# Performance work log

Measured on AMD Instinct MI355X. Metric: run time of the kernel, lower is better.

## Reference

```python
import jax, jax.numpy as jnp
import numpy as np

BERT_DIM = 768
N_ROWS = 5
N_COLS = 12
LN_EPS = 1e-5


def setup_inputs() -> dict:
    key = jax.random.key(0)
    ks = jax.random.split(key, 12)
    B, S = 256, 512
    token_hidden = jax.random.normal(ks[0], (B, S, BERT_DIM), dtype=jnp.float32)
    attention_mask = jax.random.randint(ks[1], (B, S), 0, 2, dtype=jnp.int32)
    s = lambda fan_in: 1.0 / np.sqrt(fan_in)
    return {
        "token_hidden": token_hidden,
        "attention_mask": attention_mask,
        # token_attention: Linear(768,128) -> Tanh -> Linear(128,1)
        "att_w1": jax.random.normal(ks[2], (128, BERT_DIM), dtype=jnp.float32) * s(BERT_DIM),
        "att_b1": jnp.zeros((128,), dtype=jnp.float32),
        "att_w2": jax.random.normal(ks[3], (1, 128), dtype=jnp.float32) * s(128),
        "att_b2": jnp.zeros((1,), dtype=jnp.float32),
        # feature_projector: Linear(768,256) -> GELU -> Dropout(eval) -> Linear(256,5)
        "proj_w1": jax.random.normal(ks[4], (256, BERT_DIM), dtype=jnp.float32) * s(BERT_DIM),
        "proj_b1": jnp.zeros((256,), dtype=jnp.float32),
        "proj_w2": jax.random.normal(ks[5], (N_ROWS, 256), dtype=jnp.float32) * s(256),
        "proj_b2": jnp.zeros((N_ROWS,), dtype=jnp.float32),
        # LayerNorm([5, 12])
        "ln_gamma": jnp.ones((N_ROWS, N_COLS), dtype=jnp.float32),
        "ln_beta": jnp.zeros((N_ROWS, N_COLS), dtype=jnp.float32),
    }


def reference(token_hidden, attention_mask, att_w1, att_b1, att_w2, att_b2,
              proj_w1, proj_b1, proj_w2, proj_b2, ln_gamma, ln_beta):
    # token attention scores: [B, S]
    h = jnp.tanh(jnp.einsum("bsd,hd->bsh", token_hidden, att_w1) + att_b1)
    scores = (jnp.einsum("bsh,oh->bso", h, att_w2) + att_b2)[..., 0]
    scores = jnp.where(attention_mask == 0, jnp.finfo(scores.dtype).min, scores)
    weights = jax.nn.softmax(scores, axis=-1)
    # top-k token selection (indices sorted ascending to preserve order)
    k = min(N_COLS, token_hidden.shape[1])
    _, top_idx = jax.lax.top_k(weights, k)  # [B, k]
    top_idx = jnp.sort(top_idx, axis=-1)
    selected = jnp.take_along_axis(token_hidden, top_idx[:, :, None], axis=1)  # [B, k, D]
    # feature projector (dropout is eval no-op)
    f = jax.nn.gelu(jnp.einsum("bkd,hd->bkh", selected, proj_w1) + proj_b1, approximate=False)
    f = jnp.einsum("bkh,rh->bkr", f, proj_w2) + proj_b2  # [B, k, n_rows]
    features = jnp.transpose(f, (0, 2, 1))  # [B, n_rows, k]
    if features.shape[-1] < N_COLS:
        features = jnp.pad(features, ((0, 0), (0, 0), (0, N_COLS - features.shape[-1])))
    # LayerNorm over trailing [n_rows, n_cols]
    mean = jnp.mean(features, axis=(-2, -1), keepdims=True)
    var = jnp.var(features, axis=(-2, -1), keepdims=True)
    return ln_gamma * (features - mean) * jax.lax.rsqrt(var + LN_EPS) + ln_beta
```

## Files before the change

### kernel.cpp

```cpp
#include <hip/hip_runtime.h>
#include <math.h>

#define B_BATCH 256
#define S_LEN   512
#define D_DIM   768
#define H_ATT   128
#define TOPK    12
#define NCAND   16
#define H_PROJ  256
#define N_ROWS  5
#define N_COLS  12

typedef __bf16 bf16x8 __attribute__((ext_vector_type(8)));
typedef float  f32x4  __attribute__((ext_vector_type(4)));

#define WS_SCORES 0
#define WS_WHI    524288
#define WS_WLO    720896
#define WS_W1Q    917504
#define WS_W1P    1310720

__global__ __launch_bounds__(256) void prep_kernel(
    const float* __restrict__ w1,
    const float* __restrict__ pw1,
    __bf16* __restrict__ whi, __bf16* __restrict__ wlo,
    float* __restrict__ w1q, float* __restrict__ w1p)
{
    int id = blockIdx.x * 256 + threadIdx.x;
    if (id < 98304) {
        int j    = id & 7;
        int lane = (id >> 3) & 63;
        int rest = id >> 9;
        int kt   = rest % 24;
        int nt   = rest / 24;
        int n = nt * 16 + (lane & 15);
        int k = kt * 32 + (lane >> 4) * 8 + j;
        float f = w1[n * D_DIM + k];
        __bf16 h = (__bf16)f;
        whi[id] = h;
        wlo[id] = (__bf16)(f - (float)h);
    } else if (id < 196608) {
        int e2 = id - 98304;
        int i  = e2 & 3;
        int n  = (e2 >> 2) & 127;
        int k4 = e2 >> 9;
        w1q[e2] = w1[n * D_DIM + k4 * 4 + i];
    } else {
        int e  = id - 196608;
        int i  = e & 3;
        int j  = (e >> 2) & 255;
        int k4 = e >> 10;
        w1p[e] = pw1[j * D_DIM + k4 * 4 + i];
    }
}

__device__ inline void split8(float4 a, float4 b, bf16x8& hi, bf16x8& lo) {
    float v[8] = {a.x, a.y, a.z, a.w, b.x, b.y, b.z, b.w};
#pragma unroll
    for (int i = 0; i < 8; ++i) {
        __bf16 h = (__bf16)v[i];
        hi[i] = h;
        lo[i] = (__bf16)(v[i] - (float)h);
    }
}

__global__ __launch_bounds__(256) void score_mfma(
    const float*  __restrict__ th,
    const __bf16* __restrict__ whi,
    const __bf16* __restrict__ wlo,
    const float*  __restrict__ b1,
    const float*  __restrict__ w2,
    float* __restrict__ scores)
{
    const int ln = threadIdx.x & 63;
    const int gw = (blockIdx.x * 256 + threadIdx.x) >> 6;

    const size_t row0 = (size_t)gw * 32 + (ln & 15);
    const float* pa0 = th + row0 * D_DIM + (ln >> 4) * 8;
    const float* pa1 = pa0 + 16 * D_DIM;

    f32x4 acc[2][8];
    const f32x4 z = {0.f, 0.f, 0.f, 0.f};
#pragma unroll
    for (int i = 0; i < 2; ++i)
#pragma unroll
        for (int j = 0; j < 8; ++j) acc[i][j] = z;

    float4 c00 = *(const float4*)(pa0);
    float4 c01 = *(const float4*)(pa0 + 4);
    float4 c10 = *(const float4*)(pa1);
    float4 c11 = *(const float4*)(pa1 + 4);

    for (int kt = 0; kt < 24; ++kt) {
        const int ktn = (kt < 23) ? kt + 1 : 23;
        float4 n00 = *(const float4*)(pa0 + ktn * 32);
        float4 n01 = *(const float4*)(pa0 + ktn * 32 + 4);
        float4 n10 = *(const float4*)(pa1 + ktn * 32);
        float4 n11 = *(const float4*)(pa1 + ktn * 32 + 4);

        bf16x8 ah0, al0, ah1, al1;
        split8(c00, c01, ah0, al0);
        split8(c10, c11, ah1, al1);

        const __bf16* bhp = whi + ((size_t)kt * 64 + ln) * 8;
        const __bf16* blp = wlo + ((size_t)kt * 64 + ln) * 8;
#pragma unroll
        for (int nt = 0; nt < 8; ++nt) {
            bf16x8 bh = *(const bf16x8*)(bhp + (size_t)nt * 24 * 512);
            bf16x8 bl = *(const bf16x8*)(blp + (size_t)nt * 24 * 512);
            acc[0][nt] = __builtin_amdgcn_mfma_f32_16x16x32_bf16(ah0, bh, acc[0][nt], 0, 0, 0);
            acc[0][nt] = __builtin_amdgcn_mfma_f32_16x16x32_bf16(al0, bh, acc[0][nt], 0, 0, 0);
            acc[0][nt] = __builtin_amdgcn_mfma_f32_16x16x32_bf16(ah0, bl, acc[0][nt], 0, 0, 0);
            acc[1][nt] = __builtin_amdgcn_mfma_f32_16x16x32_bf16(ah1, bh, acc[1][nt], 0, 0, 0);
            acc[1][nt] = __builtin_amdgcn_mfma_f32_16x16x32_bf16(al1, bh, acc[1][nt], 0, 0, 0);
            acc[1][nt] = __builtin_amdgcn_mfma_f32_16x16x32_bf16(ah1, bl, acc[1][nt], 0, 0, 0);
        }
        c00 = n00; c01 = n01; c10 = n10; c11 = n11;
    }

    const int col = ln & 15;
    float b1v[8], w2v[8];
#pragma unroll
    for (int nt = 0; nt < 8; ++nt) {
        b1v[nt] = b1[nt * 16 + col];
        w2v[nt] = w2[nt * 16 + col];
    }
#pragma unroll
    for (int mf = 0; mf < 2; ++mf)
#pragma unroll
        for (int r = 0; r < 4; ++r) {
            float s = 0.f;
#pragma unroll
            for (int nt = 0; nt < 8; ++nt)
                s += tanhf(acc[mf][nt][r] + b1v[nt]) * w2v[nt];
            s += __shfl_xor(s, 1, 64);
            s += __shfl_xor(s, 2, 64);
            s += __shfl_xor(s, 4, 64);
            s += __shfl_xor(s, 8, 64);
            if (col == 0)
                scores[(size_t)gw * 32 + mf * 16 + (ln >> 4) * 4 + r] = s;
        }
}

__global__ __launch_bounds__(256) void select_kernel(
    const float* __restrict__ th,
    const int*   __restrict__ mask,
    const float* __restrict__ ascores,
    const float* __restrict__ w1q,
    const float* __restrict__ ab1,
    const float* __restrict__ aw2,
    const float* __restrict__ w1p,
    const float* __restrict__ pb1,
    const float* __restrict__ pw2,
    const float* __restrict__ pb2,
    const float* __restrict__ gamma,
    const float* __restrict__ beta,
    float* __restrict__ out)
{
    const int b   = blockIdx.x;
    const int tid = threadIdx.x;
    const int wv  = tid >> 6;
    const int ln  = tid & 63;

    __shared__ float4 xc[NCAND][192];
    __shared__ unsigned long long wtop[64];
    __shared__ int   cand[NCAND];
    __shared__ float redW[4][8];
    __shared__ float exact_sc[NCAND];
    __shared__ int   sel_slot[TOPK];
    __shared__ float gbuf[TOPK][H_PROJ + 1];
    __shared__ float feat[N_ROWS * N_COLS];
    __shared__ float stats[2];

    const float NEG_MIN = -3.402823466e38f;

    {
        int i0 = wv * 128 + ln, i1 = i0 + 64;
        float v0 = ascores[(size_t)b * S_LEN + i0];
        if (mask[(size_t)b * S_LEN + i0] == 0) v0 = NEG_MIN;
        float v1 = ascores[(size_t)b * S_LEN + i1];
        if (mask[(size_t)b * S_LEN + i1] == 0) v1 = NEG_MIN;
        unsigned k0 = __float_as_uint(v0);
        k0 = ((int)k0 >= 0) ? (k0 | 0x80000000u) : ~k0;
        unsigned k1 = __float_as_uint(v1);
        k1 = ((int)k1 >= 0) ? (k1 | 0x80000000u) : ~k1;
        unsigned long long p0 = ((unsigned long long)k0 << 32) | (0xFFFFFFFFu - (unsigned)i0);
        unsigned long long p1 = ((unsigned long long)k1 << 32) | (0xFFFFFFFFu - (unsigned)i1);
        for (int it = 0; it < NCAND; ++it) {
            unsigned long long m = p0 > p1 ? p0 : p1;
#pragma unroll
            for (int s = 1; s <= 32; s <<= 1) {
                unsigned long long o = __shfl_xor(m, s, 64);
                if (o > m) m = o;
            }
            if (ln == 0) wtop[wv * 16 + it] = m;
            if (p0 == m) p0 = 0ull;
            else if (p1 == m) p1 = 0ull;
        }
    }
    __syncthreads();
    if (wv == 0) {
        unsigned long long q = wtop[ln];
        for (int it = 0; it < NCAND; ++it) {
            unsigned long long m = q;
#pragma unroll
            for (int s = 1; s <= 32; s <<= 1) {
                unsigned long long o = __shfl_xor(m, s, 64);
                if (o > m) m = o;
            }
            if (ln == 0) cand[it] = (int)(0xFFFFFFFFu - (unsigned)(m & 0xFFFFFFFFu));
            if (q == m) q = 0ull;
        }
    }
    __syncthreads();

#pragma unroll
    for (int i = 0; i < 12; ++i) {
        int f = tid + 256 * i;
        int c = f / 192, k4 = f % 192;
        xc[c][k4] = *(const float4*)(th + ((size_t)b * S_LEN + cand[c]) * D_DIM + k4 * 4);
    }
    __syncthreads();

    {
        const int n = tid & 127;
        const int h = tid >> 7;
        float accs[8];
#pragma unroll
        for (int ci = 0; ci < 8; ++ci) accs[ci] = 0.f;
        for (int k4 = 0; k4 < 192; ++k4) {
            float4 w = *(const float4*)(w1q + (size_t)(k4 * 128 + n) * 4);
#pragma unroll
            for (int ci = 0; ci < 8; ++ci) {
                float4 x = xc[2 * ci + h][k4];
                accs[ci] += w.x * x.x + w.y * x.y + w.z * x.z + w.w * x.w;
            }
        }
        float b1n = ab1[n], w2n = aw2[n];
#pragma unroll
        for (int ci = 0; ci < 8; ++ci) {
            float val = tanhf(accs[ci] + b1n) * w2n;
            val += __shfl_xor(val, 1, 64);
            val += __shfl_xor(val, 2, 64);
            val += __shfl_xor(val, 4, 64);
            val += __shfl_xor(val, 8, 64);
            val += __shfl_xor(val, 16, 64);
            val += __shfl_xor(val, 32, 64);
            if (ln == 0) redW[wv][ci] = val;
        }
    }
    __syncthreads();
    if (tid < NCAND) {
        int c = tid;
        float ex = (c & 1) ? (redW[2][c >> 1] + redW[3][c >> 1])
                           : (redW[0][c >> 1] + redW[1][c >> 1]);
        if (mask[(size_t)b * S_LEN + cand[c]] == 0) ex = -INFINITY;
        exact_sc[c] = ex;
    }
    __syncthreads();

    if (tid == 0) {
        unsigned picked = 0;
        int slots[TOPK];
        for (int it = 0; it < TOPK; ++it) {
            float best = -INFINITY; int bslot = -1; int bidx = 1 << 30;
            for (int c = 0; c < NCAND; ++c) {
                if (picked & (1u << c)) continue;
                float e = exact_sc[c]; int idx = cand[c];
                if (e > best || (e == best && idx < bidx)) { best = e; bslot = c; bidx = idx; }
            }
            picked |= 1u << bslot;
            slots[it] = bslot;
        }
        for (int i = 1; i < TOPK; ++i) {
            int s = slots[i], key = cand[s], j = i - 1;
            while (j >= 0 && cand[slots[j]] > key) { slots[j + 1] = slots[j]; --j; }
            slots[j + 1] = s;
        }
        for (int t = 0; t < TOPK; ++t) sel_slot[t] = slots[t];
    }
    __syncthreads();

    {
        const int c0 = wv * 3;
        int s0 = sel_slot[c0], s1 = sel_slot[c0 + 1], s2 = sel_slot[c0 + 2];
        float accp[4][3];
#pragma unroll
        for (int cc = 0; cc < 4; ++cc) {
            float bj = pb1[cc * 64 + ln];
            accp[cc][0] = bj; accp[cc][1] = bj; accp[cc][2] = bj;
        }
        for (int k4 = 0; k4 < 192; ++k4) {
            float4 x0 = xc[s0][k4];
            float4 x1 = xc[s1][k4];
            float4 x2 = xc[s2][k4];
#pragma unroll
            for (int cc = 0; cc < 4; ++cc) {
                float4 w = *(const float4*)(w1p + (size_t)(k4 * 256 + cc * 64 + ln) * 4);
                accp[cc][0] += w.x * x0.x + w.y * x0.y + w.z * x0.z + w.w * x0.w;
                accp[cc][1] += w.x * x1.x + w.y * x1.y + w.z * x1.z + w.w * x1.w;
                accp[cc][2] += w.x * x2.x + w.y * x2.y + w.z * x2.z + w.w * x2.w;
            }
        }
#pragma unroll
        for (int cc = 0; cc < 4; ++cc)
#pragma unroll
            for (int c = 0; c < 3; ++c) {
                float hh = accp[cc][c];
                gbuf[c0 + c][cc * 64 + ln] =
                    0.5f * hh * (1.0f + erff(hh * 0.70710678118654752f));
            }
    }
    __syncthreads();

    if (tid < TOPK * N_ROWS) {
        int t = tid / N_ROWS, r = tid % N_ROWS;
        float s = pb2[r];
        for (int j = 0; j < H_PROJ; ++j) s += gbuf[t][j] * pw2[r * H_PROJ + j];
        feat[r * N_COLS + t] = s;
    }
    __syncthreads();

    if (tid == 0) {
        float sum = 0.f;
        for (int i = 0; i < N_ROWS * N_COLS; ++i) sum += feat[i];
        float mean = sum / 60.f;
        float sq = 0.f;
        for (int i = 0; i < N_ROWS * N_COLS; ++i) { float d = feat[i] - mean; sq += d * d; }
        stats[0] = mean;
        stats[1] = sq / 60.f;
    }
    __syncthreads();
    if (tid < N_ROWS * N_COLS) {
        float x = feat[tid];
        out[(size_t)b * 60 + tid] =
            gamma[tid] * (x - stats[0]) * rsqrtf(stats[1] + 1e-5f) + beta[tid];
    }
}

extern "C" void kernel_launch(void* const* d_in, const int* in_sizes, int n_in,
                              void* d_out, int out_size, void* d_ws, size_t ws_size,
                              hipStream_t stream) {
    const float* th   = (const float*)d_in[0];
    const int*   mask = (const int*)  d_in[1];
    const float* aw1  = (const float*)d_in[2];
    const float* ab1  = (const float*)d_in[3];
    const float* aw2  = (const float*)d_in[4];
    const float* pw1  = (const float*)d_in[6];
    const float* pb1  = (const float*)d_in[7];
    const float* pw2  = (const float*)d_in[8];
    const float* pb2  = (const float*)d_in[9];
    const float* gam  = (const float*)d_in[10];
    const float* bet  = (const float*)d_in[11];
    float* out = (float*)d_out;

    char* ws = (char*)d_ws;
    float*  scores = (float*)(ws + WS_SCORES);
    __bf16* whi    = (__bf16*)(ws + WS_WHI);
    __bf16* wlo    = (__bf16*)(ws + WS_WLO);
    float*  w1q    = (float*)(ws + WS_W1Q);
    float*  w1p    = (float*)(ws + WS_W1P);

    hipLaunchKernelGGL(prep_kernel, dim3(1536), dim3(256), 0, stream,
                       aw1, pw1, whi, wlo, w1q, w1p);
    hipLaunchKernelGGL(score_mfma, dim3(1024), dim3(256), 0, stream,
                       th, whi, wlo, ab1, aw2, scores);
    hipLaunchKernelGGL(select_kernel, dim3(B_BATCH), dim3(256), 0, stream,
                       th, mask, scores, w1q, ab1, aw2,
                       w1p, pb1, pw2, pb2, gam, bet, out);
}
```

Measured before the change: 792.5 us.

## Stage score-GEMM weights in LDS via async loads; retile projector loop

The score kernel now makes each 4-wave block cooperatively stage the bf16 hi/lo weight tiles into double-buffered LDS using global_load_lds. This replaces the per-wave global weight reads, so the four waves share one copy and global traffic for B drops. A block barrier is added every k-step, and launch bounds now request 4 blocks per CU. In the select kernel, each thread now owns one hidden unit across all 12 selected tokens, so every w1p weight is loaded once instead of once per wave. The second projection layer is vectorised with float4 reads, for which the gbuf padding is changed to keep rows 16-byte aligned.

```diff
diff --git a/kernel.cpp b/kernel.cpp
--- a/kernel.cpp
+++ b/kernel.cpp
@@ -13,6 +13,9 @@
 
 typedef __bf16 bf16x8 __attribute__((ext_vector_type(8)));
 typedef float  f32x4  __attribute__((ext_vector_type(4)));
+
+#define GLOBAL_AS __attribute__((address_space(1)))
+#define LDS_AS    __attribute__((address_space(3)))
 
 #define WS_SCORES 0
 #define WS_WHI    524288
@@ -64,7 +67,7 @@
     }
 }
 
-__global__ __launch_bounds__(256) void score_mfma(
+__global__ __launch_bounds__(256, 4) void score_mfma(
     const float*  __restrict__ th,
     const __bf16* __restrict__ whi,
     const __bf16* __restrict__ wlo,
@@ -72,12 +75,29 @@
     const float*  __restrict__ w2,
     float* __restrict__ scores)
 {
-    const int ln = threadIdx.x & 63;
-    const int gw = (blockIdx.x * 256 + threadIdx.x) >> 6;
-
-    const size_t row0 = (size_t)gw * 32 + (ln & 15);
+    __shared__ __bf16 Bs[2][2][8 * 512];
+
+    const int tid = threadIdx.x;
+    const int wv  = tid >> 6;
+    const int ln  = tid & 63;
+
+    const size_t row0 = (size_t)blockIdx.x * 128 + wv * 32 + (ln & 15);
     const float* pa0 = th + row0 * D_DIM + (ln >> 4) * 8;
     const float* pa1 = pa0 + 16 * D_DIM;
+
+    auto stage = [&](int kt, int buf) {
+#pragma unroll
+        for (int q = 0; q < 4; ++q) {
+            int s  = wv + q * 4;
+            int hl = s >> 3;
+            int nt = s & 7;
+            const __bf16* src = (hl ? wlo : whi) +
+                                (((size_t)nt * 24 + kt) * 64 + ln) * 8;
+            __bf16* dst = &Bs[buf][hl][nt * 512];
+            __builtin_amdgcn_global_load_lds(
+                (GLOBAL_AS const void*)src, (LDS_AS void*)dst, 16, 0, 0);
+        }
+    };
 
     f32x4 acc[2][8];
     const f32x4 z = {0.f, 0.f, 0.f, 0.f};
@@ -90,24 +110,28 @@
     float4 c01 = *(const float4*)(pa0 + 4);
     float4 c10 = *(const float4*)(pa1);
     float4 c11 = *(const float4*)(pa1 + 4);
+    stage(0, 0);
+    __syncthreads();
 
     for (int kt = 0; kt < 24; ++kt) {
-        const int ktn = (kt < 23) ? kt + 1 : 23;
-        float4 n00 = *(const float4*)(pa0 + ktn * 32);
-        float4 n01 = *(const float4*)(pa0 + ktn * 32 + 4);
-        float4 n10 = *(const float4*)(pa1 + ktn * 32);
-        float4 n11 = *(const float4*)(pa1 + ktn * 32 + 4);
+        const int buf = kt & 1;
+        float4 n00, n01, n10, n11;
+        if (kt < 23) {
+            n00 = *(const float4*)(pa0 + (kt + 1) * 32);
+            n01 = *(const float4*)(pa0 + (kt + 1) * 32 + 4);
+            n10 = *(const float4*)(pa1 + (kt + 1) * 32);
+            n11 = *(const float4*)(pa1 + (kt + 1) * 32 + 4);
+            stage(kt + 1, buf ^ 1);
+        }
 
         bf16x8 ah0, al0, ah1, al1;
         split8(c00, c01, ah0, al0);
         split8(c10, c11, ah1, al1);
 
-        const __bf16* bhp = whi + ((size_t)kt * 64 + ln) * 8;
-        const __bf16* blp = wlo + ((size_t)kt * 64 + ln) * 8;
 #pragma unroll
         for (int nt = 0; nt < 8; ++nt) {
-            bf16x8 bh = *(const bf16x8*)(bhp + (size_t)nt * 24 * 512);
-            bf16x8 bl = *(const bf16x8*)(blp + (size_t)nt * 24 * 512);
+            bf16x8 bh = *(bf16x8*)(&Bs[buf][0][nt * 512 + ln * 8]);
+            bf16x8 bl = *(bf16x8*)(&Bs[buf][1][nt * 512 + ln * 8]);
             acc[0][nt] = __builtin_amdgcn_mfma_f32_16x16x32_bf16(ah0, bh, acc[0][nt], 0, 0, 0);
             acc[0][nt] = __builtin_amdgcn_mfma_f32_16x16x32_bf16(al0, bh, acc[0][nt], 0, 0, 0);
             acc[0][nt] = __builtin_amdgcn_mfma_f32_16x16x32_bf16(ah0, bl, acc[0][nt], 0, 0, 0);
@@ -115,7 +139,10 @@
             acc[1][nt] = __builtin_amdgcn_mfma_f32_16x16x32_bf16(al1, bh, acc[1][nt], 0, 0, 0);
             acc[1][nt] = __builtin_amdgcn_mfma_f32_16x16x32_bf16(ah1, bl, acc[1][nt], 0, 0, 0);
         }
-        c00 = n00; c01 = n01; c10 = n10; c11 = n11;
+        if (kt < 23) {
+            c00 = n00; c01 = n01; c10 = n10; c11 = n11;
+            __syncthreads();
+        }
     }
 
     const int col = ln & 15;
@@ -125,6 +152,7 @@
         b1v[nt] = b1[nt * 16 + col];
         w2v[nt] = w2[nt * 16 + col];
     }
+    const size_t rowbase = (size_t)blockIdx.x * 128 + wv * 32;
 #pragma unroll
     for (int mf = 0; mf < 2; ++mf)
 #pragma unroll
@@ -138,7 +166,7 @@
             s += __shfl_xor(s, 4, 64);
             s += __shfl_xor(s, 8, 64);
             if (col == 0)
-                scores[(size_t)gw * 32 + mf * 16 + (ln >> 4) * 4 + r] = s;
+                scores[rowbase + mf * 16 + (ln >> 4) * 4 + r] = s;
         }
 }
 
@@ -168,7 +196,7 @@
     __shared__ float redW[4][8];
     __shared__ float exact_sc[NCAND];
     __shared__ int   sel_slot[TOPK];
-    __shared__ float gbuf[TOPK][H_PROJ + 1];
+    __shared__ float gbuf[TOPK][H_PROJ + 4];
     __shared__ float feat[N_ROWS * N_COLS];
     __shared__ float stats[2];
 
@@ -282,41 +310,39 @@
     __syncthreads();
 
     {
-        const int c0 = wv * 3;
-        int s0 = sel_slot[c0], s1 = sel_slot[c0 + 1], s2 = sel_slot[c0 + 2];
-        float accp[4][3];
-#pragma unroll
-        for (int cc = 0; cc < 4; ++cc) {
-            float bj = pb1[cc * 64 + ln];
-            accp[cc][0] = bj; accp[cc][1] = bj; accp[cc][2] = bj;
-        }
+        const int j = tid;
+        int slots[TOPK];
+#pragma unroll
+        for (int t = 0; t < TOPK; ++t) slots[t] = sel_slot[t];
+        float accp[TOPK];
+        float bj = pb1[j];
+#pragma unroll
+        for (int t = 0; t < TOPK; ++t) accp[t] = bj;
         for (int k4 = 0; k4 < 192; ++k4) {
-            float4 x0 = xc[s0][k4];
-            float4 x1 = xc[s1][k4];
-            float4 x2 = xc[s2][k4];
-#pragma unroll
-            for (int cc = 0; cc < 4; ++cc) {
-                float4 w = *(const float4*)(w1p + (size_t)(k4 * 256 + cc * 64 + ln) * 4);
-                accp[cc][0] += w.x * x0.x + w.y * x0.y + w.z * x0.z + w.w * x0.w;
-                accp[cc][1] += w.x * x1.x + w.y * x1.y + w.z * x1.z + w.w * x1.w;
-                accp[cc][2] += w.x * x2.x + w.y * x2.y + w.z * x2.z + w.w * x2.w;
-            }
-        }
-#pragma unroll
-        for (int cc = 0; cc < 4; ++cc)
-#pragma unroll
-            for (int c = 0; c < 3; ++c) {
-                float hh = accp[cc][c];
-                gbuf[c0 + c][cc * 64 + ln] =
-                    0.5f * hh * (1.0f + erff(hh * 0.70710678118654752f));
-            }
+            float4 w = *(const float4*)(w1p + ((size_t)k4 * 256 + j) * 4);
+#pragma unroll
+            for (int t = 0; t < TOPK; ++t) {
+                float4 x = xc[slots[t]][k4];
+                accp[t] += w.x * x.x + w.y * x.y + w.z * x.z + w.w * x.w;
+            }
+        }
+#pragma unroll
+        for (int t = 0; t < TOPK; ++t) {
+            float hh = accp[t];
+            gbuf[t][j] = 0.5f * hh * (1.0f + erff(hh * 0.70710678118654752f));
+        }
     }
     __syncthreads();
 
     if (tid < TOPK * N_ROWS) {
         int t = tid / N_ROWS, r = tid % N_ROWS;
         float s = pb2[r];
-        for (int j = 0; j < H_PROJ; ++j) s += gbuf[t][j] * pw2[r * H_PROJ + j];
+        const float4* gp = (const float4*)&gbuf[t][0];
+        const float4* wp = (const float4*)(pw2 + r * H_PROJ);
+        for (int q = 0; q < H_PROJ / 4; ++q) {
+            float4 g = gp[q], w = wp[q];
+            s += g.x * w.x + g.y * w.y + g.z * w.z + g.w * w.w;
+        }
         feat[r * N_COLS + t] = s;
     }
     __syncthreads();
```

Measured after the change: 727.7 us. 1.09x faster.
